# Kernel tuning notes

Hardware: AMD Instinct MI355X
Metric: run time of the kernel (lower is better)

## Reference

```python
import jax, jax.numpy as jnp
import numpy as np

SEQ_LEN = 70      # hardcoded in original (view(-1, 70))
HIDDEN = 230
EMB = 50
VOCAB = 100000
BIG_NUM = 64
N_TOTAL = 2048
N_REL = 100       # hardcoded relation count
POS_VOCAB = 123
POS_DIM = 5
D_IN = EMB + 2 * POS_DIM


def setup_inputs() -> dict:
    key = jax.random.key(0)
    ks = jax.random.split(key, 20)
    bag = N_TOTAL // BIG_NUM
    labels = jax.random.randint(ks[3], (BIG_NUM,), 0, N_REL)
    inp = {
        "sentence": jax.random.randint(ks[0], (N_TOTAL, SEQ_LEN), 0, VOCAB),
        "pos1": jax.random.randint(ks[1], (N_TOTAL, SEQ_LEN), 0, POS_VOCAB),
        "pos2": jax.random.randint(ks[2], (N_TOTAL, SEQ_LEN), 0, POS_VOCAB),
        "total_shape": jnp.arange(BIG_NUM + 1, dtype=jnp.int32) * bag,
        "y_batch": jax.nn.one_hot(labels, N_REL, dtype=jnp.float32),
        "word_emb": jax.random.normal(ks[4], (VOCAB, EMB), jnp.float32) * 0.1,
        "pos1_table": jax.random.normal(ks[5], (POS_VOCAB, POS_DIM), jnp.float32) * 0.1,
        "pos2_table": jax.random.normal(ks[6], (POS_VOCAB, POS_DIM), jnp.float32) * 0.1,
        "W_ih_f": jax.random.normal(ks[7], (3 * HIDDEN, D_IN), jnp.float32) * 0.05,
        "W_hh_f": jax.random.normal(ks[8], (3 * HIDDEN, HIDDEN), jnp.float32) * 0.05,
        "b_ih_f": jnp.zeros((3 * HIDDEN,), jnp.float32),
        "b_hh_f": jnp.zeros((3 * HIDDEN,), jnp.float32),
        "W_ih_b": jax.random.normal(ks[9], (3 * HIDDEN, D_IN), jnp.float32) * 0.05,
        "W_hh_b": jax.random.normal(ks[10], (3 * HIDDEN, HIDDEN), jnp.float32) * 0.05,
        "b_ih_b": jnp.zeros((3 * HIDDEN,), jnp.float32),
        "b_hh_b": jnp.zeros((3 * HIDDEN,), jnp.float32),
        "attention_w": jax.random.normal(ks[11], (HIDDEN, 1), jnp.float32) * 0.1,
        "sen_a": jax.random.normal(ks[12], (HIDDEN,), jnp.float32) * 0.1,
        "sen_r": jax.random.normal(ks[13], (HIDDEN, 1), jnp.float32) * 0.1,
        "relation_embedding": jax.random.normal(ks[14], (N_REL, HIDDEN), jnp.float32) * 0.1,
        "sen_d": jax.random.normal(ks[15], (N_REL,), jnp.float32) * 0.1,
    }
    return inp


def _gru_dir(x_proj, W_hh, b_hh, reverse):
    """One GRU direction. x_proj: [N,T,3H] = x @ W_ih^T + b_ih (precomputed)."""
    N = x_proj.shape[0]
    H = W_hh.shape[1]

    def step(h, gi):
        gh = h @ W_hh.T + b_hh
        i_r, i_z, i_n = jnp.split(gi, 3, axis=-1)
        h_r, h_z, h_n = jnp.split(gh, 3, axis=-1)
        r = jax.nn.sigmoid(i_r + h_r)
        z = jax.nn.sigmoid(i_z + h_z)
        n = jnp.tanh(i_n + r * h_n)
        h = (1.0 - z) * n + z * h
        return h, h

    h0 = jnp.zeros((N, H), x_proj.dtype)
    _, ys = jax.lax.scan(step, h0, jnp.swapaxes(x_proj, 0, 1), reverse=reverse)
    return jnp.swapaxes(ys, 0, 1)  # [N,T,H]


def reference(sentence, pos1, pos2, total_shape, y_batch,
              word_emb, pos1_table, pos2_table,
              W_ih_f, W_hh_f, b_ih_f, b_hh_f,
              W_ih_b, W_hh_b, b_ih_b, b_hh_b,
              attention_w, sen_a, sen_r, relation_embedding, sen_d):
    # embedding lookup + concat -> [N, T, D_IN]
    emb = jnp.concatenate([word_emb[sentence], pos1_table[pos1], pos2_table[pos2]], axis=-1)
    gi_f = jnp.einsum('ntd,gd->ntg', emb, W_ih_f) + b_ih_f
    gi_b = jnp.einsum('ntd,gd->ntg', emb, W_ih_b) + b_ih_b
    # bidirectional GRU, then sum fwd + bwd halves (torch.add(tupf, tupb))
    tup = _gru_dir(gi_f, W_hh_f, b_hh_f, False) + _gru_dir(gi_b, W_hh_b, b_hh_b, True)  # [N,T,H]
    # word-level attention over the 70 timesteps
    word_alpha = jax.nn.softmax((jnp.tanh(tup) @ attention_w)[..., 0], axis=-1)  # [N,T]
    attention_r = jnp.einsum('nt,nth->nh', word_alpha, tup)                       # [N,H]
    repre = jnp.tanh(attention_r)
    # ragged per-bag (sentence-level) attention via segment ops
    n_total = repre.shape[0]
    seg = jnp.searchsorted(total_shape[1:], jnp.arange(n_total), side='right')   # [N] bag ids
    s = ((repre * sen_a) @ sen_r)[:, 0]                                          # [N]
    m = jax.ops.segment_max(s, seg, num_segments=BIG_NUM)
    e = jnp.exp(s - m[seg])
    denom = jax.ops.segment_sum(e, seg, num_segments=BIG_NUM)
    alpha = e / denom[seg]
    sen_s = jax.ops.segment_sum(alpha[:, None] * repre, seg, num_segments=BIG_NUM)  # [B,H]
    logits = sen_s @ relation_embedding.T + sen_d                                   # [B,100]
    prob = jax.nn.softmax(logits, axis=-1)
    # BCEWithLogitsLoss (mean over 100 classes) summed over bags
    bce = jnp.maximum(logits, 0.0) - logits * y_batch + jnp.log1p(jnp.exp(-jnp.abs(logits)))
    total_loss = jnp.sum(jnp.mean(bce, axis=-1))
    acc = (jnp.argmax(prob, axis=-1) == jnp.argmax(y_batch, axis=-1)).astype(jnp.float32)
    return total_loss, acc, prob
```

## Files before the change

### kernel.cpp

```cpp
#include <hip/hip_runtime.h>
#include <hip/hip_bf16.h>
#include <math.h>

#define SEQ 70
#define HID 230
#define G3  690
#define EMBD 50
#define DIN 60
#define NTOT 2048
#define NREL 100
#define NBAG 64
#define BAGSZ 32
#define PDIM 5
#define MB 8


__global__ void k_zero(float* p, long n) {
    long i = (long)blockIdx.x * 256 + threadIdx.x;
    if (i < n) p[i] = 0.f;
}

__global__ void k_embed(const int* __restrict__ sent, const int* __restrict__ p1,
                        const int* __restrict__ p2,  const float* __restrict__ wemb,
                        const float* __restrict__ t1, const float* __restrict__ t2,
                        float* __restrict__ emb) {
    long idx = (long)blockIdx.x * 256 + threadIdx.x;
    long total = (long)NTOT * SEQ * DIN;
    if (idx >= total) return;
    int nt = (int)(idx / DIN);
    int j  = (int)(idx % DIN);
    float v;
    if (j < EMBD)            v = wemb[(long)sent[nt] * EMBD + j];
    else if (j < EMBD + PDIM) v = t1[p1[nt] * PDIM + (j - EMBD)];
    else                      v = t2[p2[nt] * PDIM + (j - EMBD - PDIM)];
    emb[idx] = v;
}

__global__ void k_transpose(const float* __restrict__ in, float* __restrict__ out,
                            int G, int K) {
    int idx = blockIdx.x * 256 + threadIdx.x;
    if (idx >= G * K) return;
    int g = idx / K, k = idx % K;
    out[k * G + g] = in[idx];
}

__global__ __launch_bounds__(256) void k_gru(
    const float* __restrict__ emb,
    const float* __restrict__ wihT_f, const float* __restrict__ whhT_f,
    const float* __restrict__ bih_f,  const float* __restrict__ bhh_f,
    const float* __restrict__ wihT_b, const float* __restrict__ whhT_b,
    const float* __restrict__ bih_b,  const float* __restrict__ bhh_b,
    float* __restrict__ tup) {

    const bool rev = blockIdx.x & 1;
    const int  n0  = (blockIdx.x >> 1) * MB;
    const float* wihT = rev ? wihT_b : wihT_f;
    const float* whhT = rev ? whhT_b : whhT_f;
    const float* bih  = rev ? bih_b  : bih_f;
    const float* bhh  = rev ? bhh_b  : bhh_f;
    const int tid = threadIdx.x;

    __shared__ float h_s[HID * MB];
    __shared__ float e_s[DIN * MB];
    __shared__ float P_s[G3 * MB];
    __shared__ float Q_s[HID * MB];

    for (int i = tid; i < HID * MB; i += 256) h_s[i] = 0.f;

    const int g0 = tid;
    const int g1 = tid + 256;
    const int g2 = tid + 512;
    const bool v2 = (g2 < G3);

    const float bi0 = bih[g0], bh0 = bhh[g0];
    const float bi1 = bih[g1], bh1 = bhh[g1];
    const float bi2 = v2 ? bih[g2] : 0.f, bh2 = v2 ? bhh[g2] : 0.f;

    for (int t = 0; t < SEQ; ++t) {
        const int tt = rev ? (SEQ - 1 - t) : t;

        for (int i = tid; i < DIN * MB; i += 256) {
            int n = i / DIN, k = i - n * DIN;
            e_s[k * MB + n] = emb[((long)(n0 + n) * SEQ + tt) * DIN + k];
        }
        __syncthreads();

        float a0[MB], a1[MB], a2[MB], h0[MB], h1[MB], h2[MB];
#pragma unroll
        for (int n = 0; n < MB; ++n) {
            a0[n] = bi0; a1[n] = bi1; a2[n] = bi2;
            h0[n] = bh0; h1[n] = bh1; h2[n] = bh2;
        }
        for (int k = 0; k < DIN; ++k) {
            float w0 = wihT[k * G3 + g0];
            float w1 = wihT[k * G3 + g1];
            float w2 = v2 ? wihT[k * G3 + g2] : 0.f;
            const float4* ep = (const float4*)&e_s[k * MB];
            float4 ea = ep[0], eb = ep[1];
            float ev[8] = {ea.x, ea.y, ea.z, ea.w, eb.x, eb.y, eb.z, eb.w};
#pragma unroll
            for (int n = 0; n < MB; ++n) {
                a0[n] = fmaf(w0, ev[n], a0[n]);
                a1[n] = fmaf(w1, ev[n], a1[n]);
                a2[n] = fmaf(w2, ev[n], a2[n]);
            }
        }
        for (int k = 0; k < HID; ++k) {
            float w0 = whhT[k * G3 + g0];
            float w1 = whhT[k * G3 + g1];
            float w2 = v2 ? whhT[k * G3 + g2] : 0.f;
            const float4* hp = (const float4*)&h_s[k * MB];
            float4 ha = hp[0], hb = hp[1];
            float hv[8] = {ha.x, ha.y, ha.z, ha.w, hb.x, hb.y, hb.z, hb.w};
#pragma unroll
            for (int n = 0; n < MB; ++n) {
                h0[n] = fmaf(w0, hv[n], h0[n]);
                h1[n] = fmaf(w1, hv[n], h1[n]);
                h2[n] = fmaf(w2, hv[n], h2[n]);
            }
        }
#pragma unroll
        for (int n = 0; n < MB; ++n) P_s[g0 * MB + n] = a0[n] + h0[n];
        if (g1 < 2 * HID) {
#pragma unroll
            for (int n = 0; n < MB; ++n) P_s[g1 * MB + n] = a1[n] + h1[n];
        } else {
#pragma unroll
            for (int n = 0; n < MB; ++n) {
                P_s[g1 * MB + n] = a1[n];
                Q_s[(g1 - 2 * HID) * MB + n] = h1[n];
            }
        }
        if (v2) {
#pragma unroll
            for (int n = 0; n < MB; ++n) {
                P_s[g2 * MB + n] = a2[n];
                Q_s[(g2 - 2 * HID) * MB + n] = h2[n];
            }
        }
        __syncthreads();

        for (int e = tid; e < HID * MB; e += 256) {
            int n = e / HID, hh = e - n * HID;
            int idx = hh * MB + n;
            float r = 1.f / (1.f + expf(-P_s[idx]));
            float z = 1.f / (1.f + expf(-P_s[(HID + hh) * MB + n]));
            float nn = tanhf(P_s[(2 * HID + hh) * MB + n] + r * Q_s[idx]);
            float hold = h_s[idx];
            float hnew = (1.f - z) * nn + z * hold;
            h_s[idx] = hnew;
            atomicAdd(&tup[((long)(n0 + n) * SEQ + tt) * HID + hh], hnew);
        }
    }
}

__global__ __launch_bounds__(256) void k_wordattn(
    const float* __restrict__ tup, const float* __restrict__ attw,
    const float* __restrict__ sen_a, const float* __restrict__ sen_r,
    float* __restrict__ repre, float* __restrict__ sbuf) {
    const int n = blockIdx.x, tid = threadIdx.x;
    __shared__ float tl[SEQ * HID];
    __shared__ float sc[SEQ];
    __shared__ float red[4];
    for (int i = tid; i < SEQ * HID; i += 256) tl[i] = tup[(long)n * SEQ * HID + i];
    __syncthreads();
    if (tid < SEQ) {
        float s = 0.f;
        for (int h = 0; h < HID; ++h) s += tanhf(tl[tid * HID + h]) * attw[h];
        sc[tid] = s;
    }
    __syncthreads();
    if (tid == 0) {
        float m = sc[0];
        for (int t = 1; t < SEQ; ++t) m = fmaxf(m, sc[t]);
        float ssum = 0.f;
        for (int t = 0; t < SEQ; ++t) { float e = expf(sc[t] - m); sc[t] = e; ssum += e; }
        float inv = 1.f / ssum;
        for (int t = 0; t < SEQ; ++t) sc[t] *= inv;
    }
    __syncthreads();
    float part = 0.f;
    if (tid < HID) {
        float r = 0.f;
        for (int t = 0; t < SEQ; ++t) r = fmaf(sc[t], tl[t * HID + tid], r);
        float rep = tanhf(r);
        repre[(long)n * HID + tid] = rep;
        part = rep * sen_a[tid] * sen_r[tid];
    }
    for (int off = 32; off; off >>= 1) part += __shfl_down(part, off, 64);
    if ((tid & 63) == 0) red[tid >> 6] = part;
    __syncthreads();
    if (tid == 0) sbuf[n] = red[0] + red[1] + red[2] + red[3];
}

__global__ __launch_bounds__(256) void k_bag(
    const float* __restrict__ repre, const float* __restrict__ sbuf,
    const float* __restrict__ rel, const float* __restrict__ sen_d,
    const float* __restrict__ y, float* __restrict__ out, float* __restrict__ bagloss) {
    const int b = blockIdx.x, tid = threadIdx.x;
    __shared__ float al[BAGSZ];
    __shared__ float ss[HID];
    __shared__ float lg[NREL];
    if (tid == 0) {
        float m = -1e30f;
        for (int i = 0; i < BAGSZ; ++i) m = fmaxf(m, sbuf[b * BAGSZ + i]);
        float s = 0.f;
        for (int i = 0; i < BAGSZ; ++i) { float e = expf(sbuf[b * BAGSZ + i] - m); al[i] = e; s += e; }
        float inv = 1.f / s;
        for (int i = 0; i < BAGSZ; ++i) al[i] *= inv;
    }
    __syncthreads();
    if (tid < HID) {
        float acc = 0.f;
        for (int i = 0; i < BAGSZ; ++i)
            acc = fmaf(al[i], repre[(long)(b * BAGSZ + i) * HID + tid], acc);
        ss[tid] = acc;
    }
    __syncthreads();
    if (tid < NREL) {
        float acc = sen_d[tid];
        for (int h = 0; h < HID; ++h) acc = fmaf(ss[h], rel[tid * HID + h], acc);
        lg[tid] = acc;
    }
    __syncthreads();
    if (tid == 0) {
        float m = -1e30f; int am = 0;
        for (int r = 0; r < NREL; ++r) if (lg[r] > m) { m = lg[r]; am = r; }
        float s = 0.f;
        for (int r = 0; r < NREL; ++r) s += expf(lg[r] - m);
        float inv = 1.f / s;
        float ym = -1e30f; int ay = 0;
        for (int r = 0; r < NREL; ++r) { float yy = y[b * NREL + r]; if (yy > ym) { ym = yy; ay = r; } }
        out[1 + b] = (am == ay) ? 1.f : 0.f;
        float loss = 0.f;
        for (int r = 0; r < NREL; ++r) {
            float l = lg[r], yy = y[b * NREL + r];
            loss += fmaxf(l, 0.f) - l * yy + log1pf(expf(-fabsf(l)));
            out[1 + NBAG + b * NREL + r] = expf(l - m) * inv;
        }
        bagloss[b] = loss / NREL;
    }
}

__global__ void k_final(const float* __restrict__ bagloss, float* __restrict__ out) {
    if (blockIdx.x == 0 && threadIdx.x == 0) {
        float s = 0.f;
        for (int i = 0; i < NBAG; ++i) s += bagloss[i];
        out[0] = s;
    }
}

extern "C" void kernel_launch(void* const* d_in, const int* in_sizes, int n_in,
                              void* d_out, int out_size, void* d_ws, size_t ws_size,
                              hipStream_t stream) {
    const int*   sent   = (const int*)d_in[0];
    const int*   pos1   = (const int*)d_in[1];
    const int*   pos2   = (const int*)d_in[2];
    const float* ybatch = (const float*)d_in[4];
    const float* wemb   = (const float*)d_in[5];
    const float* p1tab  = (const float*)d_in[6];
    const float* p2tab  = (const float*)d_in[7];
    const float* Wih_f  = (const float*)d_in[8];
    const float* Whh_f  = (const float*)d_in[9];
    const float* bih_f  = (const float*)d_in[10];
    const float* bhh_f  = (const float*)d_in[11];
    const float* Wih_b  = (const float*)d_in[12];
    const float* Whh_b  = (const float*)d_in[13];
    const float* bih_b  = (const float*)d_in[14];
    const float* bhh_b  = (const float*)d_in[15];
    const float* attw   = (const float*)d_in[16];
    const float* sen_a  = (const float*)d_in[17];
    const float* sen_r  = (const float*)d_in[18];
    const float* rel    = (const float*)d_in[19];
    const float* sen_d  = (const float*)d_in[20];
    float* out = (float*)d_out;

    float* ws = (float*)d_ws;
    size_t off = 0;
    float* emb    = ws + off; off += (size_t)NTOT * SEQ * DIN;
    float* wihT_f = ws + off; off += (size_t)DIN * G3;
    float* wihT_b = ws + off; off += (size_t)DIN * G3;
    float* whhT_f = ws + off; off += (size_t)HID * G3;
    float* whhT_b = ws + off; off += (size_t)HID * G3;
    float* tup    = ws + off; off += (size_t)NTOT * SEQ * HID;
    float* repre  = ws + off; off += (size_t)NTOT * HID;
    float* sbuf   = ws + off; off += (size_t)NTOT;
    float* bagloss= ws + off; off += (size_t)NBAG;

    const long tupN = (long)NTOT * SEQ * HID;
    k_zero<<<(int)((tupN + 255) / 256), 256, 0, stream>>>(tup, tupN);

    const long embN = (long)NTOT * SEQ * DIN;
    k_embed<<<(int)((embN + 255) / 256), 256, 0, stream>>>(sent, pos1, pos2, wemb, p1tab, p2tab, emb);

    k_transpose<<<(G3 * DIN + 255) / 256, 256, 0, stream>>>(Wih_f, wihT_f, G3, DIN);
    k_transpose<<<(G3 * DIN + 255) / 256, 256, 0, stream>>>(Wih_b, wihT_b, G3, DIN);
    k_transpose<<<(G3 * HID + 255) / 256, 256, 0, stream>>>(Whh_f, whhT_f, G3, HID);
    k_transpose<<<(G3 * HID + 255) / 256, 256, 0, stream>>>(Whh_b, whhT_b, G3, HID);

    k_gru<<<(NTOT / MB) * 2, 256, 0, stream>>>(emb,
        wihT_f, whhT_f, bih_f, bhh_f,
        wihT_b, whhT_b, bih_b, bhh_b, tup);

    k_wordattn<<<NTOT, 256, 0, stream>>>(tup, attw, sen_a, sen_r, repre, sbuf);

    k_bag<<<NBAG, 256, 0, stream>>>(repre, sbuf, rel, sen_d, ybatch, out, bagloss);

    k_final<<<1, 64, 0, stream>>>(bagloss, out);
}
```

Before: 2.915 ms.

## Assign one hidden unit per thread in GRU and fuse gate math into registers

Restructures the GRU step so each thread owns one hidden unit and computes its r, z, and n gate pre-activations for all batch rows. The gate nonlinearities and state update then happen in registers without the P_s/Q_s shared staging and one barrier per step. Hidden state is double-buffered in shared memory, and the embedding load is vectorized with float4. Only 230 of 256 threads do useful work, and atomic stores to the output remain.

```diff
diff --git a/kernel.cpp b/kernel.cpp
--- a/kernel.cpp
+++ b/kernel.cpp
@@ -12,7 +12,7 @@
 #define NBAG 64
 #define BAGSZ 32
 #define PDIM 5
-#define MB 8
+#define MBS 8
 
 
 __global__ void k_zero(float* p, long n) {
@@ -30,7 +30,7 @@
     int nt = (int)(idx / DIN);
     int j  = (int)(idx % DIN);
     float v;
-    if (j < EMBD)            v = wemb[(long)sent[nt] * EMBD + j];
+    if (j < EMBD)             v = wemb[(long)sent[nt] * EMBD + j];
     else if (j < EMBD + PDIM) v = t1[p1[nt] * PDIM + (j - EMBD)];
     else                      v = t2[p2[nt] * PDIM + (j - EMBD - PDIM)];
     emb[idx] = v;
@@ -53,103 +53,106 @@
     float* __restrict__ tup) {
 
     const bool rev = blockIdx.x & 1;
-    const int  n0  = (blockIdx.x >> 1) * MB;
+    const int  n0  = (blockIdx.x >> 1) * MBS;
     const float* wihT = rev ? wihT_b : wihT_f;
     const float* whhT = rev ? whhT_b : whhT_f;
     const float* bih  = rev ? bih_b  : bih_f;
     const float* bhh  = rev ? bhh_b  : bhh_f;
     const int tid = threadIdx.x;
 
-    __shared__ float h_s[HID * MB];
-    __shared__ float e_s[DIN * MB];
-    __shared__ float P_s[G3 * MB];
-    __shared__ float Q_s[HID * MB];
-
-    for (int i = tid; i < HID * MB; i += 256) h_s[i] = 0.f;
-
-    const int g0 = tid;
-    const int g1 = tid + 256;
-    const int g2 = tid + 512;
-    const bool v2 = (g2 < G3);
-
-    const float bi0 = bih[g0], bh0 = bhh[g0];
-    const float bi1 = bih[g1], bh1 = bhh[g1];
-    const float bi2 = v2 ? bih[g2] : 0.f, bh2 = v2 ? bhh[g2] : 0.f;
+    __shared__ float h_s[2][HID * MBS];
+    __shared__ float e_s[2][DIN * MBS];
+
+    for (int i = tid; i < HID * MBS; i += 256) h_s[0][i] = 0.f;
+
+    const int  hh  = tid;
+    const bool act = (hh < HID);
+    const int  c_r = act ? hh           : 0;
+    const int  c_z = act ? (HID + hh)   : 0;
+    const int  c_n = act ? (2*HID + hh) : 0;
+
+    const float brz0 = act ? (bih[c_r] + bhh[c_r]) : 0.f;
+    const float bzz0 = act ? (bih[c_z] + bhh[c_z]) : 0.f;
+    const float bin0 = act ? bih[c_n] : 0.f;
+    const float bhn0 = act ? bhh[c_n] : 0.f;
+
+    const float* wir = wihT + c_r;
+    const float* wiz = wihT + c_z;
+    const float* win = wihT + c_n;
+    const float* whr = whhT + c_r;
+    const float* whz = whhT + c_z;
+    const float* whn = whhT + c_n;
+
+    float hprev[MBS];
+#pragma unroll
+    for (int n = 0; n < MBS; ++n) hprev[n] = 0.f;
 
     for (int t = 0; t < SEQ; ++t) {
-        const int tt = rev ? (SEQ - 1 - t) : t;
-
-        for (int i = tid; i < DIN * MB; i += 256) {
-            int n = i / DIN, k = i - n * DIN;
-            e_s[k * MB + n] = emb[((long)(n0 + n) * SEQ + tt) * DIN + k];
+        const int tt  = rev ? (SEQ - 1 - t) : t;
+        const int cur = t & 1, nxt = cur ^ 1;
+
+        if (tid < 120) {
+            int n = tid / 15, q = tid - n * 15;
+            const float4 v = *(const float4*)&emb[((long)(n0 + n) * SEQ + tt) * DIN + q * 4];
+            int k = q * 4;
+            e_s[cur][(k + 0) * MBS + n] = v.x;
+            e_s[cur][(k + 1) * MBS + n] = v.y;
+            e_s[cur][(k + 2) * MBS + n] = v.z;
+            e_s[cur][(k + 3) * MBS + n] = v.w;
         }
         __syncthreads();
 
-        float a0[MB], a1[MB], a2[MB], h0[MB], h1[MB], h2[MB];
-#pragma unroll
-        for (int n = 0; n < MB; ++n) {
-            a0[n] = bi0; a1[n] = bi1; a2[n] = bi2;
-            h0[n] = bh0; h1[n] = bh1; h2[n] = bh2;
-        }
+        float ar[MBS], az[MBS], ain[MBS], ahn[MBS];
+#pragma unroll
+        for (int n = 0; n < MBS; ++n) {
+            ar[n] = brz0; az[n] = bzz0; ain[n] = bin0; ahn[n] = bhn0;
+        }
+
+#pragma unroll 4
         for (int k = 0; k < DIN; ++k) {
-            float w0 = wihT[k * G3 + g0];
-            float w1 = wihT[k * G3 + g1];
-            float w2 = v2 ? wihT[k * G3 + g2] : 0.f;
-            const float4* ep = (const float4*)&e_s[k * MB];
-            float4 ea = ep[0], eb = ep[1];
-            float ev[8] = {ea.x, ea.y, ea.z, ea.w, eb.x, eb.y, eb.z, eb.w};
-#pragma unroll
-            for (int n = 0; n < MB; ++n) {
-                a0[n] = fmaf(w0, ev[n], a0[n]);
-                a1[n] = fmaf(w1, ev[n], a1[n]);
-                a2[n] = fmaf(w2, ev[n], a2[n]);
+            float wr = wir[(size_t)k * G3];
+            float wz = wiz[(size_t)k * G3];
+            float wn = win[(size_t)k * G3];
+            const float4* ep = (const float4*)&e_s[cur][k * MBS];
+            float4 e0 = ep[0], e1 = ep[1];
+            float ev[MBS] = {e0.x, e0.y, e0.z, e0.w, e1.x, e1.y, e1.z, e1.w};
+#pragma unroll
+            for (int n = 0; n < MBS; ++n) {
+                ar[n]  = fmaf(wr, ev[n], ar[n]);
+                az[n]  = fmaf(wz, ev[n], az[n]);
+                ain[n] = fmaf(wn, ev[n], ain[n]);
             }
         }
+#pragma unroll 5
         for (int k = 0; k < HID; ++k) {
-            float w0 = whhT[k * G3 + g0];
-            float w1 = whhT[k * G3 + g1];
-            float w2 = v2 ? whhT[k * G3 + g2] : 0.f;
-            const float4* hp = (const float4*)&h_s[k * MB];
-            float4 ha = hp[0], hb = hp[1];
-            float hv[8] = {ha.x, ha.y, ha.z, ha.w, hb.x, hb.y, hb.z, hb.w};
-#pragma unroll
-            for (int n = 0; n < MB; ++n) {
-                h0[n] = fmaf(w0, hv[n], h0[n]);
-                h1[n] = fmaf(w1, hv[n], h1[n]);
-                h2[n] = fmaf(w2, hv[n], h2[n]);
+            float wr = whr[(size_t)k * G3];
+            float wz = whz[(size_t)k * G3];
+            float wn = whn[(size_t)k * G3];
+            const float4* hp = (const float4*)&h_s[cur][k * MBS];
+            float4 x0 = hp[0], x1 = hp[1];
+            float hv[MBS] = {x0.x, x0.y, x0.z, x0.w, x1.x, x1.y, x1.z, x1.w};
+#pragma unroll
+            for (int n = 0; n < MBS; ++n) {
+                ar[n]  = fmaf(wr, hv[n], ar[n]);
+                az[n]  = fmaf(wz, hv[n], az[n]);
+                ahn[n] = fmaf(wn, hv[n], ahn[n]);
             }
         }
-#pragma unroll
-        for (int n = 0; n < MB; ++n) P_s[g0 * MB + n] = a0[n] + h0[n];
-        if (g1 < 2 * HID) {
-#pragma unroll
-            for (int n = 0; n < MB; ++n) P_s[g1 * MB + n] = a1[n] + h1[n];
-        } else {
-#pragma unroll
-            for (int n = 0; n < MB; ++n) {
-                P_s[g1 * MB + n] = a1[n];
-                Q_s[(g1 - 2 * HID) * MB + n] = h1[n];
+
+        if (act) {
+            float hnew[MBS];
+#pragma unroll
+            for (int n = 0; n < MBS; ++n) {
+                float r  = 1.f / (1.f + expf(-ar[n]));
+                float z  = 1.f / (1.f + expf(-az[n]));
+                float nn = tanhf(ain[n] + r * ahn[n]);
+                hnew[n] = (1.f - z) * nn + z * hprev[n];
+                hprev[n] = hnew[n];
+                h_s[nxt][hh * MBS + n] = hnew[n];
             }
-        }
-        if (v2) {
-#pragma unroll
-            for (int n = 0; n < MB; ++n) {
-                P_s[g2 * MB + n] = a2[n];
-                Q_s[(g2 - 2 * HID) * MB + n] = h2[n];
-            }
-        }
-        __syncthreads();
-
-        for (int e = tid; e < HID * MB; e += 256) {
-            int n = e / HID, hh = e - n * HID;
-            int idx = hh * MB + n;
-            float r = 1.f / (1.f + expf(-P_s[idx]));
-            float z = 1.f / (1.f + expf(-P_s[(HID + hh) * MB + n]));
-            float nn = tanhf(P_s[(2 * HID + hh) * MB + n] + r * Q_s[idx]);
-            float hold = h_s[idx];
-            float hnew = (1.f - z) * nn + z * hold;
-            h_s[idx] = hnew;
-            atomicAdd(&tup[((long)(n0 + n) * SEQ + tt) * HID + hh], hnew);
+#pragma unroll
+            for (int n = 0; n < MBS; ++n)
+                atomicAdd(&tup[((long)(n0 + n) * SEQ + tt) * HID + hh], hnew[n]);
         }
     }
 }
@@ -298,7 +301,7 @@
     k_transpose<<<(G3 * HID + 255) / 256, 256, 0, stream>>>(Whh_f, whhT_f, G3, HID);
     k_transpose<<<(G3 * HID + 255) / 256, 256, 0, stream>>>(Whh_b, whhT_b, G3, HID);
 
-    k_gru<<<(NTOT / MB) * 2, 256, 0, stream>>>(emb,
+    k_gru<<<(NTOT / MBS) * 2, 256, 0, stream>>>(emb,
         wihT_f, whhT_f, bih_f, bhh_f,
         wihT_b, whhT_b, bih_b, bhh_b, tup);
 
```

Result: slower. 3.352 ms (+15.0%).
